# Performance work log

Hardware: AMD Instinct MI355X
Metric: run time of the kernel (lower is better)

The kernel has to match this reference:

```python
import jax, jax.numpy as jnp
import numpy as np

NEG_SLOPE = 0.01  # torch F.leaky_relu default

def _lrelu(x):
    return jax.nn.leaky_relu(x, NEG_SLOPE)

def setup_inputs() -> dict:
    key = jax.random.key(0)
    ks = jax.random.split(key, 24)
    B, N, E = 512, 20000, 640000
    n_enc_1, n_enc_2, n_z = 512, 256, 64
    n_dec_2, n_dec_1, hidden = 256, 512, 256
    p = lambda k, shp, fan: jax.random.normal(k, shp, jnp.float32) * (1.0 / np.sqrt(fan))
    return {
        "data": jax.random.normal(ks[0], (B, N), jnp.float32),
        "noise": jax.random.normal(ks[1], (B, N), jnp.float32),
        "edge_index": jax.random.randint(ks[2], (2, E), 0, N, jnp.int32),
        "w_gcn": jax.random.normal(ks[3], (), jnp.float32),
        "b_gcn": jax.random.normal(ks[4], (), jnp.float32) * 0.1,
        "enc1_w": p(ks[5], (N, n_enc_1), N), "enc1_b": p(ks[6], (n_enc_1,), N),
        "enc2_w": p(ks[7], (n_enc_1, n_enc_2), n_enc_1), "enc2_b": p(ks[8], (n_enc_2,), n_enc_1),
        "enc3_w": p(ks[9], (n_enc_2, n_z), n_enc_2), "enc3_b": p(ks[10], (n_z,), n_enc_2),
        "dec1_w": p(ks[11], (n_z, n_dec_2), n_z), "dec1_b": p(ks[12], (n_dec_2,), n_z),
        "dec2_w": p(ks[13], (n_dec_2, n_dec_1), n_dec_2), "dec2_b": p(ks[14], (n_dec_1,), n_dec_2),
        "dec3_w": p(ks[15], (n_dec_1, N), n_dec_1), "dec3_b": p(ks[16], (N,), n_dec_1),
        "disc1_w": p(ks[17], (n_z, hidden), n_z), "disc1_b": p(ks[18], (hidden,), n_z),
        "disc2_w": p(ks[19], (hidden, hidden), hidden), "disc2_b": p(ks[20], (hidden,), hidden),
        "disc3_w": p(ks[21], (hidden, 1), hidden), "disc3_b": p(ks[22], (1,), hidden),
    }

def _gcn_batched(x, edge_index, w_gcn, b_gcn):
    # x: [B, N] -> GCNConv(1,1, improved=True) applied per row, vectorized.
    B, N = x.shape
    src, dst = edge_index[0], edge_index[1]
    loop = jnp.arange(N, dtype=src.dtype)
    src_a = jnp.concatenate([src, loop])
    dst_a = jnp.concatenate([dst, loop])
    # improved=True: self-loop edge weight 2.0
    ew = jnp.concatenate([jnp.ones(src.shape[0], x.dtype), jnp.full((N,), 2.0, x.dtype)])
    deg = jax.ops.segment_sum(ew, dst_a, num_segments=N)
    dinv = jnp.where(deg > 0, jax.lax.rsqrt(deg), 0.0)
    norm = dinv[src_a] * ew * dinv[dst_a]  # [E+N]
    xl = x * w_gcn                         # lin (1x1 weight, no bias)
    msgs = xl[:, src_a] * norm[None, :]    # [B, E+N]
    agg = jnp.zeros_like(x).at[:, dst_a].add(msgs)
    return agg + b_gcn

def reference(data, noise, edge_index, w_gcn, b_gcn,
              enc1_w, enc1_b, enc2_w, enc2_b, enc3_w, enc3_b,
              dec1_w, dec1_b, dec2_w, dec2_b, dec3_w, dec3_b,
              disc1_w, disc1_b, disc2_w, disc2_b, disc3_w, disc3_b):
    x = data + noise * 0.1
    gcn_out = _lrelu(_gcn_batched(x, edge_index, w_gcn, b_gcn))  # [B, N]
    h1 = _lrelu(gcn_out @ enc1_w + enc1_b)
    h2 = _lrelu(h1 @ enc2_w + enc2_b)
    z = _lrelu(h2 @ enc3_w + enc3_b)
    d1 = _lrelu(z @ dec1_w + dec1_b)
    d2 = _lrelu(d1 @ dec2_w + dec2_b)
    dec_h3 = _lrelu(d2 @ dec3_w + dec3_b)
    g1 = _lrelu(z @ disc1_w + disc1_b)
    g2 = _lrelu(g1 @ disc2_w + disc2_b)
    d = jax.nn.sigmoid(g2 @ disc3_w + disc3_b)
    return (dec_h3, z, d)
```

## Files before the change

kernel.cpp:

```cpp
#include <hip/hip_runtime.h>
#include <hip/hip_bf16.h>


#define LRELU(v) ((v) > 0.f ? (v) : 0.01f * (v))

static constexpr int Bb = 512;
static constexpr int Nn = 20000;
static constexpr int Ee = 640000;
static constexpr int KPAD = 20480;
static constexpr int LSTR = 144;

typedef __attribute__((ext_vector_type(8))) short short8;
typedef __attribute__((ext_vector_type(4))) float f32x4;

__device__ __forceinline__ ushort f2bf(float f) {
  uint u = __builtin_bit_cast(uint, f);
  u = u + 0x7FFFu + ((u >> 16) & 1u);
  return (ushort)(u >> 16);
}
__device__ __forceinline__ float bfLo(uint u) {
  return __builtin_bit_cast(float, u << 16);
}
__device__ __forceinline__ float bfHi(uint u) {
  return __builtin_bit_cast(float, u & 0xffff0000u);
}

__global__ void transpose_xs_k(const float* __restrict__ a, const float* __restrict__ nz,
                               const float* __restrict__ dinv, ushort* __restrict__ xs, int b0) {
  __shared__ ushort tile[64][65];
  int c0 = blockIdx.x * 64;
  int p = blockIdx.y;
  int chunk = p >> 1;
  int sub = (p & 1) * 64;
  int rbase = b0 + p * 64;
  for (int i = threadIdx.x; i < 64 * 64; i += 256) {
    int rr = i >> 6, cc = i & 63;
    int r = rbase + rr, c = c0 + cc;
    ushort v = 0;
    if (c < Nn) {
      size_t idx = (size_t)r * Nn + c;
      v = f2bf(dinv[c] * (a[idx] + 0.1f * nz[idx]));
    }
    tile[rr][cc] = v;
  }
  __syncthreads();
  for (int i = threadIdx.x; i < 64 * 64; i += 256) {
    int cc = i >> 6, rr = i & 63;
    int c = c0 + cc;
    if (c < Nn) xs[(size_t)chunk * Nn * 128 + (size_t)c * 128 + sub + rr] = tile[rr][cc];
  }
}

__global__ void hist_check_k(const int* __restrict__ src, const int* __restrict__ dst, int E,
                             int* __restrict__ cnt, int* __restrict__ flag) {
  int i = blockIdx.x * 256 + threadIdx.x;
  if (i < E) {
    int s = src[i], d = dst[i];
    if ((unsigned)s >= (unsigned)Nn || (unsigned)d >= (unsigned)Nn) {
      atomicExch(flag, 1);
    } else {
      atomicAdd(&cnt[d], 1);
    }
  }
}

__global__ void offs_k(const int* __restrict__ cnt, int* __restrict__ offs,
                       int* __restrict__ cursor, float* __restrict__ dinv,
                       int* __restrict__ bump) {
  int i = blockIdx.x * 256 + threadIdx.x;
  int l = threadIdx.x & 63;
  int v = (i < Nn) ? cnt[i] : 0;
  int x = v;
#pragma unroll
  for (int d = 1; d < 64; d <<= 1) {
    int t = __shfl_up(x, d);
    if (l >= d) x += t;
  }
  int total = __shfl(x, 63);
  int base = 0;
  if (l == 0) base = atomicAdd(bump, total);
  base = __shfl(base, 0);
  int excl = base + x - v;
  if (i < Nn) {
    offs[i] = excl;
    cursor[i] = excl;
    dinv[i] = rsqrtf(2.0f + (float)v);
  }
}

__global__ void scatter_k(const int* __restrict__ src, const int* __restrict__ dst, int E,
                          int* __restrict__ cursor, uint* __restrict__ eOff) {
  int i = blockIdx.x * 256 + threadIdx.x;
  if (i < E) {
    int s = src[i], d = dst[i];
    if ((unsigned)s >= (unsigned)Nn || (unsigned)d >= (unsigned)Nn) return;
    int p = atomicAdd(&cursor[d], 1);
    eOff[p] = (uint)s * 256u;
  }
}

__global__ __launch_bounds__(256) void spmm_chunk_k(
    const ushort* __restrict__ xs, const uint* __restrict__ eOff, const int* __restrict__ offs,
    const int* __restrict__ cnt, const float* __restrict__ dinv, const float* __restrict__ wg,
    const float* __restrict__ bg, ushort* __restrict__ gcnT, int NC) {
  __shared__ uint sIdx[4][64];
  int bid = blockIdx.x;
  int chunk = bid % NC;
  int ngrp = bid / NC;
  int wv = threadIdx.x >> 6, l = threadIdx.x & 63;
  int n = ngrp * 4 + wv;
  int o = offs[n], c = cnt[n];
  const char* base = (const char*)(xs + (size_t)chunk * Nn * 128) + l * 4;
  const uint* ep = eOff + o;
  uint su = *(const uint*)(base + (size_t)n * 256);
  float a00 = 2.0f * bfLo(su), a01 = 2.0f * bfHi(su);
  float a10 = 0.f, a11 = 0.f;

  for (int bi = 0; bi < c; bi += 64) {
    int rem = c - bi;
    if (rem > 64) rem = 64;
    sIdx[wv][l] = (l < rem) ? ep[bi + l] : 0u;
    int i = 0;
    for (; i + 8 <= rem; i += 8) {
      uint u[8];
#pragma unroll
      for (int j = 0; j < 8; ++j) u[j] = *(const uint*)(base + sIdx[wv][i + j]);
#pragma unroll
      for (int j = 0; j < 8; j += 2) {
        a00 += bfLo(u[j]);
        a01 += bfHi(u[j]);
        a10 += bfLo(u[j + 1]);
        a11 += bfHi(u[j + 1]);
      }
    }
    for (; i < rem; ++i) {
      uint u = *(const uint*)(base + sIdx[wv][i]);
      a00 += bfLo(u);
      a01 += bfHi(u);
    }
  }

  float wdn = wg[0] * dinv[n], bb = bg[0];
  float v0 = wdn * (a00 + a10) + bb;
  float v1 = wdn * (a01 + a11) + bb;
  v0 = LRELU(v0);
  v1 = LRELU(v1);
  uint pk = (uint)f2bf(v0) | ((uint)f2bf(v1) << 16);
  *(uint*)&gcnT[(size_t)chunk * KPAD * 128 + (size_t)n * 128 + 2 * l] = pk;
}

template <bool SPLITK>
__global__ __launch_bounds__(256) void mfma_gemm2(const ushort* __restrict__ AT, int lda, int pw,
                                                  size_t pstride, const float* __restrict__ B,
                                                  int ldb, int KB, int Nv, int iters,
                                                  float* __restrict__ C, int ldc,
                                                  const float* __restrict__ bias) {
  __shared__ ushort As[32 * LSTR];
  __shared__ ushort Bs[32 * LSTR];
  int n0 = blockIdx.x * 128, m0 = blockIdx.y * 128;
  int k0 = blockIdx.z * iters * 32;
  int tid = threadIdx.x;
  int kr = tid >> 4, c8 = (tid & 15) * 8;
  int l = tid & 63, w = tid >> 6;
  int wr = w >> 1, wc = w & 1;
  int lrow = l & 15, lkg = l >> 4;
  const ushort* Ap = AT + (size_t)(m0 / pw) * pstride + (m0 % pw);
  f32x4 acc[4][4] = {};

  for (int kt = 0; kt < iters; ++kt) {
    int kg = k0 + kt * 32;
    uint4 av0 = *(const uint4*)&Ap[(size_t)(kg + kr) * lda + c8];
    uint4 av1 = *(const uint4*)&Ap[(size_t)(kg + kr + 16) * lda + c8];
    uint4 bv0 = {0u, 0u, 0u, 0u}, bv1 = {0u, 0u, 0u, 0u};
    int col = n0 + c8;
    if (col < Nv) {
      if (kg + kr < KB) {
        const float4* bp = (const float4*)(B + (size_t)(kg + kr) * ldb + col);
        float4 f0 = bp[0], f1 = bp[1];
        bv0.x = (uint)f2bf(f0.x) | ((uint)f2bf(f0.y) << 16);
        bv0.y = (uint)f2bf(f0.z) | ((uint)f2bf(f0.w) << 16);
        bv0.z = (uint)f2bf(f1.x) | ((uint)f2bf(f1.y) << 16);
        bv0.w = (uint)f2bf(f1.z) | ((uint)f2bf(f1.w) << 16);
      }
      if (kg + kr + 16 < KB) {
        const float4* bp = (const float4*)(B + (size_t)(kg + kr + 16) * ldb + col);
        float4 f0 = bp[0], f1 = bp[1];
        bv1.x = (uint)f2bf(f0.x) | ((uint)f2bf(f0.y) << 16);
        bv1.y = (uint)f2bf(f0.z) | ((uint)f2bf(f0.w) << 16);
        bv1.z = (uint)f2bf(f1.x) | ((uint)f2bf(f1.y) << 16);
        bv1.w = (uint)f2bf(f1.z) | ((uint)f2bf(f1.w) << 16);
      }
    }
    __syncthreads();
    {
      int p0 = (kr & 7) * 4 + (kr >> 3);
      int p1 = ((kr + 16) & 7) * 4 + ((kr + 16) >> 3);
      *(uint4*)&As[p0 * LSTR + c8] = av0;
      *(uint4*)&As[p1 * LSTR + c8] = av1;
      *(uint4*)&Bs[p0 * LSTR + c8] = bv0;
      *(uint4*)&Bs[p1 * LSTR + c8] = bv1;
    }
    __syncthreads();
    short8 a[4], b[4];
#pragma unroll
    for (int j = 0; j < 8; ++j) {
      int pr = (4 * j + lkg) * LSTR;
#pragma unroll
      for (int mi = 0; mi < 4; ++mi) a[mi][j] = (short)As[pr + wr * 64 + mi * 16 + lrow];
#pragma unroll
      for (int nj = 0; nj < 4; ++nj) b[nj][j] = (short)Bs[pr + wc * 64 + nj * 16 + lrow];
    }
#pragma unroll
    for (int mi = 0; mi < 4; ++mi)
#pragma unroll
      for (int nj = 0; nj < 4; ++nj)
        acc[mi][nj] = __builtin_amdgcn_mfma_f32_16x16x32_bf16(a[mi], b[nj], acc[mi][nj], 0, 0, 0);
  }

#pragma unroll
  for (int mi = 0; mi < 4; ++mi)
#pragma unroll
    for (int nj = 0; nj < 4; ++nj)
#pragma unroll
      for (int r = 0; r < 4; ++r) {
        int row = m0 + wr * 64 + mi * 16 + lkg * 4 + r;
        int col = n0 + wc * 64 + nj * 16 + lrow;
        if (SPLITK) {
          atomicAdd(&C[(size_t)row * ldc + col], acc[mi][nj][r]);
        } else if (col < Nv) {
          float v = acc[mi][nj][r] + bias[col];
          C[(size_t)row * ldc + col] = LRELU(v);
        }
      }
}

__global__ __launch_bounds__(256) void tail2_k(
    const float* __restrict__ h1, const float* __restrict__ c1, const float* __restrict__ W2,
    const float* __restrict__ c2, const float* __restrict__ W3, const float* __restrict__ c3,
    const float* __restrict__ Wd1, const float* __restrict__ cd1, const float* __restrict__ Wd2,
    const float* __restrict__ cd2, const float* __restrict__ Wg1, const float* __restrict__ cg1,
    const float* __restrict__ Wg2, const float* __restrict__ cg2, const float* __restrict__ Wg3,
    const float* __restrict__ cg3, float* __restrict__ out_z, float* __restrict__ out_d,
    ushort* __restrict__ d2bfT, int BT, int b0) {
  __shared__ float s_h1[512];
  __shared__ float s_h2[256];
  __shared__ float s_z[64];
  __shared__ float s_d1[256];
  __shared__ float s_g1[256];
  __shared__ float s_g2[256];
  __shared__ float s_part[4][256];
  __shared__ float s_red[4];
  int rl = blockIdx.x;
  int rg = b0 + rl;
  int t = threadIdx.x;
  int w = t >> 6, l = t & 63;

  {
    float r0 = h1[(size_t)rl * 512 + t] + c1[t];
    float r1 = h1[(size_t)rl * 512 + t + 256] + c1[t + 256];
    s_h1[t] = LRELU(r0);
    s_h1[t + 256] = LRELU(r1);
  }
  __syncthreads();

  {
    int c4 = l * 4;
    float a0 = 0.f, a1 = 0.f, a2 = 0.f, a3 = 0.f;
#pragma unroll 8
    for (int k = w * 128; k < w * 128 + 128; ++k) {
      float4 wv = *(const float4*)&W2[(size_t)k * 256 + c4];
      float x = s_h1[k];
      a0 += x * wv.x; a1 += x * wv.y; a2 += x * wv.z; a3 += x * wv.w;
    }
    float4 pv = {a0, a1, a2, a3};
    *(float4*)&s_part[w][c4] = pv;
  }
  __syncthreads();
  s_h2[t] = LRELU(s_part[0][t] + s_part[1][t] + s_part[2][t] + s_part[3][t] + c2[t]);
  __syncthreads();

  {
    int c = t >> 2, p = t & 3;
    float a = 0.f;
#pragma unroll 8
    for (int k = p * 64; k < p * 64 + 64; ++k) a += s_h2[k] * W3[(size_t)k * 64 + c];
    s_part[p][c] = a;
  }
  __syncthreads();
  if (t < 64) {
    float v = s_part[0][t] + s_part[1][t] + s_part[2][t] + s_part[3][t] + c3[t];
    v = LRELU(v);
    s_z[t] = v;
    out_z[(size_t)rg * 64 + t] = v;
  }
  __syncthreads();

  {
    float a = 0.f;
#pragma unroll
    for (int k = 0; k < 64; ++k) a += s_z[k] * Wd1[(size_t)k * 256 + t];
    s_d1[t] = LRELU(a + cd1[t]);
  }
  {
    float a = 0.f;
#pragma unroll
    for (int k = 0; k < 64; ++k) a += s_z[k] * Wg1[(size_t)k * 256 + t];
    s_g1[t] = LRELU(a + cg1[t]);
  }
  __syncthreads();

  {
    int g = t & 127, p = t >> 7;
    int c4 = g * 4;
    float a0 = 0.f, a1 = 0.f, a2 = 0.f, a3 = 0.f;
#pragma unroll 8
    for (int k = p * 128; k < p * 128 + 128; ++k) {
      float4 wv = *(const float4*)&Wd2[(size_t)k * 512 + c4];
      float x = s_d1[k];
      a0 += x * wv.x; a1 += x * wv.y; a2 += x * wv.z; a3 += x * wv.w;
    }
    float* sp = &s_part[0][0];
    float4 pv = {a0, a1, a2, a3};
    *(float4*)&sp[p * 512 + c4] = pv;
  }
  __syncthreads();
  {
    const float* sp = &s_part[0][0];
#pragma unroll
    for (int cc = 0; cc < 2; ++cc) {
      int c = t + cc * 256;
      float v = sp[c] + sp[512 + c] + cd2[c];
      v = LRELU(v);
      d2bfT[(size_t)c * BT + rl] = f2bf(v);
    }
  }
  __syncthreads();

  {
    int c4 = l * 4;
    float a0 = 0.f, a1 = 0.f, a2 = 0.f, a3 = 0.f;
#pragma unroll 8
    for (int k = w * 64; k < w * 64 + 64; ++k) {
      float4 wv = *(const float4*)&Wg2[(size_t)k * 256 + c4];
      float x = s_g1[k];
      a0 += x * wv.x; a1 += x * wv.y; a2 += x * wv.z; a3 += x * wv.w;
    }
    float4 pv = {a0, a1, a2, a3};
    *(float4*)&s_part[w][c4] = pv;
  }
  __syncthreads();
  s_g2[t] = LRELU(s_part[0][t] + s_part[1][t] + s_part[2][t] + s_part[3][t] + cg2[t]);
  __syncthreads();

  {
    float p = s_g2[t] * Wg3[t];
#pragma unroll
    for (int o = 32; o > 0; o >>= 1) p += __shfl_down(p, o);
    if ((t & 63) == 0) s_red[t >> 6] = p;
    __syncthreads();
    if (t == 0) {
      float s = s_red[0] + s_red[1] + s_red[2] + s_red[3] + cg3[0];
      out_d[rg] = 1.f / (1.f + __expf(-s));
    }
  }
}

__global__ void sentinel_k(float* out, float val) { out[0] = val; }
__global__ void flag_sentinel_k(float* out, const int* flag) {
  if (*flag != 0) out[0] = 70000.0f;
}

extern "C" void kernel_launch(void* const* d_in, const int* in_sizes, int n_in,
                              void* d_out, int out_size, void* d_ws, size_t ws_size,
                              hipStream_t stream) {
  const float* data = (const float*)d_in[0];
  const float* noise = (const float*)d_in[1];
  const int* edge = (const int*)d_in[2];
  const int* esrc_in = edge;
  const int* edst_in = edge + Ee;
  const float* w_gcn = (const float*)d_in[3];
  const float* b_gcn = (const float*)d_in[4];
  const float* enc1_w = (const float*)d_in[5];
  const float* enc1_b = (const float*)d_in[6];
  const float* enc2_w = (const float*)d_in[7];
  const float* enc2_b = (const float*)d_in[8];
  const float* enc3_w = (const float*)d_in[9];
  const float* enc3_b = (const float*)d_in[10];
  const float* dec1_w = (const float*)d_in[11];
  const float* dec1_b = (const float*)d_in[12];
  const float* dec2_w = (const float*)d_in[13];
  const float* dec2_b = (const float*)d_in[14];
  const float* dec3_w = (const float*)d_in[15];
  const float* dec3_b = (const float*)d_in[16];
  const float* disc1_w = (const float*)d_in[17];
  const float* disc1_b = (const float*)d_in[18];
  const float* disc2_w = (const float*)d_in[19];
  const float* disc2_b = (const float*)d_in[20];
  const float* disc3_w = (const float*)d_in[21];
  const float* disc3_b = (const float*)d_in[22];

  int BT = 128;
  if (ws_size >= 48500000u) BT = 512;
  else if (ws_size >= 24392500u) BT = 256;
  int NC = BT / 128;
  if (NC < 1) NC = 1;

  char* w = (char*)d_ws;
  size_t o = 0;
  auto alloc = [&](size_t bytes) {
    size_t r = o;
    o = (o + bytes + 15) & ~(size_t)15;
    return r;
  };
  ushort* xs = (ushort*)(w + alloc((size_t)Nn * BT * 2));
  ushort* gcnT = (ushort*)(w + alloc((size_t)KPAD * BT * 2));
  float* h1 = (float*)(w + alloc((size_t)BT * 512 * 4));
  ushort* d2bfT = (ushort*)(w + alloc((size_t)512 * BT * 2));
  float* dinv = (float*)(w + alloc(Nn * 4));
  int* cnt = (int*)(w + alloc(Nn * 4));
  int* offs = (int*)(w + alloc(Nn * 4));
  int* cursor = (int*)(w + alloc(Nn * 4));
  uint* eOff = (uint*)(w + alloc(Ee * 4));
  int* flag = (int*)(w + alloc(16));

  float* outp = (float*)d_out;
  float* out_dec = outp;
  float* out_z = outp + (size_t)Bb * Nn;
  float* out_d = out_z + (size_t)Bb * 64;

  static const int expect_sizes[23] = {
      10240000, 10240000, 1280000, 1, 1,
      10240000, 512, 131072, 256, 16384, 64,
      16384, 256, 131072, 512, 10240000, 20000,
      16384, 256, 65536, 256, 256, 1};
  float host_sentinel = 0.f;
  if (n_in != 23) host_sentinel = 50000.f;
  else if (out_size != 10273280) host_sentinel = 80000.f;
  else {
    for (int i = 0; i < 23; ++i)
      if (in_sizes[i] != expect_sizes[i]) { host_sentinel = 100000.f + 1000.f * i; break; }
  }

  hipMemsetAsync(cnt, 0, Nn * sizeof(int), stream);
  hipMemsetAsync(flag, 0, 2 * sizeof(int), stream);
  hist_check_k<<<(Ee + 255) / 256, 256, 0, stream>>>(esrc_in, edst_in, Ee, cnt, flag);
  offs_k<<<(Nn + 255) / 256, 256, 0, stream>>>(cnt, offs, cursor, dinv, flag + 1);
  scatter_k<<<(Ee + 255) / 256, 256, 0, stream>>>(esrc_in, edst_in, Ee, cursor, eOff);
  hipMemsetAsync(gcnT, 0, (size_t)KPAD * BT * 2, stream);

  for (int b0 = 0; b0 < Bb; b0 += BT) {
    {
      dim3 g((Nn + 63) / 64, BT / 64);
      transpose_xs_k<<<g, 256, 0, stream>>>(data, noise, dinv, xs, b0);
    }
    spmm_chunk_k<<<(Nn / 4) * NC, 256, 0, stream>>>(xs, eOff, offs, cnt, dinv, w_gcn, b_gcn,
                                                    gcnT, NC);
    hipMemsetAsync(h1, 0, (size_t)BT * 512 * 4, stream);
    {
      dim3 g(512 / 128, BT / 128, 32);
      mfma_gemm2<true><<<g, 256, 0, stream>>>(gcnT, 128, 128, (size_t)KPAD * 128, enc1_w, 512,
                                              Nn, 512, 20, h1, 512, nullptr);
    }
    tail2_k<<<BT, 256, 0, stream>>>(h1, enc1_b, enc2_w, enc2_b, enc3_w, enc3_b, dec1_w, dec1_b,
                                    dec2_w, dec2_b, disc1_w, disc1_b, disc2_w, disc2_b, disc3_w,
                                    disc3_b, out_z, out_d, d2bfT, BT, b0);
    {
      dim3 g((Nn + 127) / 128, BT / 128, 1);
      mfma_gemm2<false><<<g, 256, 0, stream>>>(d2bfT, BT, BT, 0, dec3_w, Nn, 512, Nn, 16,
                                               out_dec + (size_t)b0 * Nn, Nn, dec3_b);
    }
  }

  flag_sentinel_k<<<1, 1, 0, stream>>>(out_dec, flag);
  if (host_sentinel != 0.f) sentinel_k<<<1, 1, 0, stream>>>(out_dec, host_sentinel);
}
```

Measured before the change: 296.1 us.

## Transpose GEMM shared-memory tiles to row-major and prefetch next K tile

The shared-memory tiles change from K-major rows with scalar 16-bit gathers to M/N-major rows padded to 36 halves. Each thread packs pairs of K values into 32-bit words, so MFMA operands can be read as two 64-bit vector loads instead of 16 scalar reads per fragment. The global loads for the next K tile are now issued after the second barrier, overlapping them with the MFMA work through register double-buffering. The cost is more registers for the prefetch buffers, extra pack instructions, and possible LDS bank conflicts on the strided 32-bit writes.

```diff
diff --git a/kernel.cpp b/kernel.cpp
--- a/kernel.cpp
+++ b/kernel.cpp
@@ -8,9 +8,11 @@
 static constexpr int Nn = 20000;
 static constexpr int Ee = 640000;
 static constexpr int KPAD = 20480;
-static constexpr int LSTR = 144;
+static constexpr int RSU = 36;
+static constexpr int RSW = 18;
 
 typedef __attribute__((ext_vector_type(8))) short short8;
+typedef __attribute__((ext_vector_type(4))) short short4v;
 typedef __attribute__((ext_vector_type(4))) float f32x4;
 
 __device__ __forceinline__ ushort f2bf(float f) {
@@ -150,65 +152,93 @@
 }
 
 template <bool SPLITK>
-__global__ __launch_bounds__(256) void mfma_gemm2(const ushort* __restrict__ AT, int lda, int pw,
+__global__ __launch_bounds__(256) void mfma_gemm3(const ushort* __restrict__ AT, int lda, int pw,
                                                   size_t pstride, const float* __restrict__ B,
                                                   int ldb, int KB, int Nv, int iters,
                                                   float* __restrict__ C, int ldc,
                                                   const float* __restrict__ bias) {
-  __shared__ ushort As[32 * LSTR];
-  __shared__ ushort Bs[32 * LSTR];
+  __shared__ ushort As[128 * RSU];
+  __shared__ ushort Bs[128 * RSU];
   int n0 = blockIdx.x * 128, m0 = blockIdx.y * 128;
   int k0 = blockIdx.z * iters * 32;
   int tid = threadIdx.x;
-  int kr = tid >> 4, c8 = (tid & 15) * 8;
+  int kp = tid >> 4;
+  int c8 = (tid & 15) * 8;
   int l = tid & 63, w = tid >> 6;
   int wr = w >> 1, wc = w & 1;
   int lrow = l & 15, lkg = l >> 4;
   const ushort* Ap = AT + (size_t)(m0 / pw) * pstride + (m0 % pw);
+  int bcol = n0 + c8;
+  bool bok = bcol < Nv;
   f32x4 acc[4][4] = {};
 
+  uint4 pa0, pa1;
+  float4 pb00, pb01, pb10, pb11;
+
+#define GLOAD(KG)                                                                       \
+  {                                                                                     \
+    int kq = (KG) + 2 * kp;                                                             \
+    pa0 = *(const uint4*)&Ap[(size_t)kq * lda + c8];                                    \
+    pa1 = *(const uint4*)&Ap[(size_t)(kq + 1) * lda + c8];                              \
+    pb00 = pb01 = pb10 = pb11 = float4{0.f, 0.f, 0.f, 0.f};                             \
+    if (bok) {                                                                          \
+      if (kq < KB) {                                                                    \
+        const float4* bp = (const float4*)(B + (size_t)kq * ldb + bcol);                \
+        pb00 = bp[0];                                                                   \
+        pb01 = bp[1];                                                                   \
+      }                                                                                 \
+      if (kq + 1 < KB) {                                                                \
+        const float4* bp = (const float4*)(B + (size_t)(kq + 1) * ldb + bcol);          \
+        pb10 = bp[0];                                                                   \
+        pb11 = bp[1];                                                                   \
+      }                                                                                 \
+    }                                                                                   \
+  }
+
+  GLOAD(k0);
+
   for (int kt = 0; kt < iters; ++kt) {
-    int kg = k0 + kt * 32;
-    uint4 av0 = *(const uint4*)&Ap[(size_t)(kg + kr) * lda + c8];
-    uint4 av1 = *(const uint4*)&Ap[(size_t)(kg + kr + 16) * lda + c8];
-    uint4 bv0 = {0u, 0u, 0u, 0u}, bv1 = {0u, 0u, 0u, 0u};
-    int col = n0 + c8;
-    if (col < Nv) {
-      if (kg + kr < KB) {
-        const float4* bp = (const float4*)(B + (size_t)(kg + kr) * ldb + col);
-        float4 f0 = bp[0], f1 = bp[1];
-        bv0.x = (uint)f2bf(f0.x) | ((uint)f2bf(f0.y) << 16);
-        bv0.y = (uint)f2bf(f0.z) | ((uint)f2bf(f0.w) << 16);
-        bv0.z = (uint)f2bf(f1.x) | ((uint)f2bf(f1.y) << 16);
-        bv0.w = (uint)f2bf(f1.z) | ((uint)f2bf(f1.w) << 16);
-      }
-      if (kg + kr + 16 < KB) {
-        const float4* bp = (const float4*)(B + (size_t)(kg + kr + 16) * ldb + col);
-        float4 f0 = bp[0], f1 = bp[1];
-        bv1.x = (uint)f2bf(f0.x) | ((uint)f2bf(f0.y) << 16);
-        bv1.y = (uint)f2bf(f0.z) | ((uint)f2bf(f0.w) << 16);
-        bv1.z = (uint)f2bf(f1.x) | ((uint)f2bf(f1.y) << 16);
-        bv1.w = (uint)f2bf(f1.z) | ((uint)f2bf(f1.w) << 16);
-      }
-    }
+    uint wa[8], wb[8];
+    wa[0] = (pa0.x & 0xffffu) | (pa1.x << 16);
+    wa[1] = (pa0.x >> 16) | (pa1.x & 0xffff0000u);
+    wa[2] = (pa0.y & 0xffffu) | (pa1.y << 16);
+    wa[3] = (pa0.y >> 16) | (pa1.y & 0xffff0000u);
+    wa[4] = (pa0.z & 0xffffu) | (pa1.z << 16);
+    wa[5] = (pa0.z >> 16) | (pa1.z & 0xffff0000u);
+    wa[6] = (pa0.w & 0xffffu) | (pa1.w << 16);
+    wa[7] = (pa0.w >> 16) | (pa1.w & 0xffff0000u);
+    wb[0] = (uint)f2bf(pb00.x) | ((uint)f2bf(pb10.x) << 16);
+    wb[1] = (uint)f2bf(pb00.y) | ((uint)f2bf(pb10.y) << 16);
+    wb[2] = (uint)f2bf(pb00.z) | ((uint)f2bf(pb10.z) << 16);
+    wb[3] = (uint)f2bf(pb00.w) | ((uint)f2bf(pb10.w) << 16);
+    wb[4] = (uint)f2bf(pb01.x) | ((uint)f2bf(pb11.x) << 16);
+    wb[5] = (uint)f2bf(pb01.y) | ((uint)f2bf(pb11.y) << 16);
+    wb[6] = (uint)f2bf(pb01.z) | ((uint)f2bf(pb11.z) << 16);
+    wb[7] = (uint)f2bf(pb01.w) | ((uint)f2bf(pb11.w) << 16);
     __syncthreads();
     {
-      int p0 = (kr & 7) * 4 + (kr >> 3);
-      int p1 = ((kr + 16) & 7) * 4 + ((kr + 16) >> 3);
-      *(uint4*)&As[p0 * LSTR + c8] = av0;
-      *(uint4*)&As[p1 * LSTR + c8] = av1;
-      *(uint4*)&Bs[p0 * LSTR + c8] = bv0;
-      *(uint4*)&Bs[p1 * LSTR + c8] = bv1;
+      uint* aw = (uint*)As;
+      uint* bw = (uint*)Bs;
+#pragma unroll
+      for (int j = 0; j < 8; ++j) {
+        aw[(c8 + j) * RSW + kp] = wa[j];
+        bw[(c8 + j) * RSW + kp] = wb[j];
+      }
     }
     __syncthreads();
+    if (kt + 1 < iters) GLOAD(k0 + (kt + 1) * 32);
     short8 a[4], b[4];
 #pragma unroll
-    for (int j = 0; j < 8; ++j) {
-      int pr = (4 * j + lkg) * LSTR;
-#pragma unroll
-      for (int mi = 0; mi < 4; ++mi) a[mi][j] = (short)As[pr + wr * 64 + mi * 16 + lrow];
-#pragma unroll
-      for (int nj = 0; nj < 4; ++nj) b[nj][j] = (short)Bs[pr + wc * 64 + nj * 16 + lrow];
+    for (int mi = 0; mi < 4; ++mi) {
+      int m = wr * 64 + mi * 16 + lrow;
+      const short4v* p = (const short4v*)&As[m * RSU + lkg * 8];
+      a[mi] = __builtin_shufflevector(p[0], p[1], 0, 1, 2, 3, 4, 5, 6, 7);
+    }
+#pragma unroll
+    for (int nj = 0; nj < 4; ++nj) {
+      int n = wc * 64 + nj * 16 + lrow;
+      const short4v* p = (const short4v*)&Bs[n * RSU + lkg * 8];
+      b[nj] = __builtin_shufflevector(p[0], p[1], 0, 1, 2, 3, 4, 5, 6, 7);
     }
 #pragma unroll
     for (int mi = 0; mi < 4; ++mi)
@@ -216,6 +246,7 @@
       for (int nj = 0; nj < 4; ++nj)
         acc[mi][nj] = __builtin_amdgcn_mfma_f32_16x16x32_bf16(a[mi], b[nj], acc[mi][nj], 0, 0, 0);
   }
+#undef GLOAD
 
 #pragma unroll
   for (int mi = 0; mi < 4; ++mi)
@@ -458,7 +489,7 @@
     hipMemsetAsync(h1, 0, (size_t)BT * 512 * 4, stream);
     {
       dim3 g(512 / 128, BT / 128, 32);
-      mfma_gemm2<true><<<g, 256, 0, stream>>>(gcnT, 128, 128, (size_t)KPAD * 128, enc1_w, 512,
+      mfma_gemm3<true><<<g, 256, 0, stream>>>(gcnT, 128, 128, (size_t)KPAD * 128, enc1_w, 512,
                                               Nn, 512, 20, h1, 512, nullptr);
     }
     tail2_k<<<BT, 256, 0, stream>>>(h1, enc1_b, enc2_w, enc2_b, enc3_w, enc3_b, dec1_w, dec1_b,
@@ -466,7 +497,7 @@
                                     disc3_b, out_z, out_d, d2bfT, BT, b0);
     {
       dim3 g((Nn + 127) / 128, BT / 128, 1);
-      mfma_gemm2<false><<<g, 256, 0, stream>>>(d2bfT, BT, BT, 0, dec3_w, Nn, 512, Nn, 16,
+      mfma_gemm3<false><<<g, 256, 0, stream>>>(d2bfT, BT, BT, 0, dec3_w, Nn, 512, Nn, 16,
                                                out_dec + (size_t)b0 * Nn, Nn, dec3_b);
     }
   }
```

Result: no change. 297.8 us (+0.6%).
